# Kernel optimization log

Measured on AMD Instinct MI355X. Metric: run time of the kernel, lower is better.

Reference implementation:

```python
import jax, jax.numpy as jnp
import numpy as np

H_D, W_D = 64, 64          # 1024x1024 image / 16 patch size
N = H_D * W_D              # 4096 patches
D = 768                    # DINO ViT-B/16 embed dim
ALPHA = 0.5
K = 100


def setup_inputs() -> dict:
    key = jax.random.key(0)
    k1, k2 = jax.random.split(key)
    out = jax.random.normal(k1, (N, D), dtype=jnp.float32)
    attn_seed = jax.random.randint(k2, (2,), 0, H_D, dtype=jnp.int32)
    return {"out": out, "attn_seed": attn_seed}


def _connected_components(mask):
    """8-connectivity connected components via iterative min-label propagation.
    Background = 0. Foreground pixels get the minimum initial id (+1) of their
    component (same partition as cv2.connectedComponents, different numbering)."""
    fg = mask > 0
    BIG = jnp.int32(N + 1)
    init = jnp.where(fg, jnp.arange(N, dtype=jnp.int32).reshape(H_D, W_D) + 1, BIG)

    def step(l):
        p = jnp.pad(l, 1, constant_values=N + 1)
        m = l
        for dy in (0, 1, 2):          # fixed 3x3 neighborhood, not a data-dim loop
            for dx in (0, 1, 2):
                m = jnp.minimum(m, p[dy:dy + H_D, dx:dx + W_D])
        return jnp.where(fg, m, BIG)

    def cond(st):
        l, prev = st
        return jnp.any(l != prev)

    def body(st):
        l, _ = st
        return step(l), l

    l, _ = jax.lax.while_loop(cond, body, (step(init), init))
    return jnp.where(fg, l, 0)


def reference(out, attn_seed):
    # similarity between all patch features: [N, N]
    sim = out @ out.T
    deg = sim >= 0                                        # degree_matrix (bool)
    # patch with fewest non-negative similarities
    seed_degree_flat = jnp.argmin(deg.sum(axis=0)).astype(jnp.int32)
    seed_degree = jnp.stack([seed_degree_flat // W_D, seed_degree_flat % W_D])
    # blend degree seed with attention seed
    seed_rc = jnp.round(ALPHA * seed_degree + (1.0 - ALPHA) * attn_seed).astype(jnp.int32)
    seed = seed_rc[0] * W_D + seed_rc[1]

    # initial expansion set = patches positively correlated with the seed
    s = deg[seed].astype(jnp.int32)
    s = s.at[seed].set(1)                                 # degree_matrix[seed][seed] = 255 (truthy)
    order = jnp.argsort(-sim[seed])                       # descending
    s = s.at[order[K:]].set(0)                            # keep top-k most similar

    # sequential seed expansion (updates feed into later iterations)
    def step(s, i):
        grows = jnp.sum(sim[i] * (s == 1)) > 0
        s = s.at[i].set(jnp.where(s[i] == 0, 0, jnp.where(grows, 1, 0)))
        return s, None

    s, _ = jax.lax.scan(step, s, jnp.arange(N))

    return _connected_components(s.reshape(H_D, W_D))
```

## Files before the change

kernel.cpp:

```cpp
#include <hip/hip_runtime.h>
#include <cstdint>

#define NP   4096
#define DD   768
#define HD   64
#define WD   64
#define KTOP 100
#define BIGL 4097

typedef short bf16x8 __attribute__((ext_vector_type(8)));
typedef float f32x4  __attribute__((ext_vector_type(4)));

__device__ __forceinline__ void gload_lds16(const void* g, void* l) {
    __builtin_amdgcn_global_load_lds(
        (const __attribute__((address_space(1))) unsigned int*)(uintptr_t)g,
        (__attribute__((address_space(3))) unsigned int*)(unsigned int)(uintptr_t)l,
        16, 0, 0);
}

__device__ __forceinline__ unsigned short f2bf_rne(float x) {
    unsigned b = __float_as_uint(x);
    unsigned r = b + 0x7FFFu + ((b >> 16) & 1u);
    return (unsigned short)(r >> 16);
}
__device__ __forceinline__ float bf2f(unsigned short h) {
    return __uint_as_float(((unsigned)h) << 16);
}

__global__ __launch_bounds__(256) void k_split(const float* __restrict__ A,
                                               unsigned short* __restrict__ hi,
                                               unsigned short* __restrict__ lo,
                                               int* __restrict__ counts) {
    if (blockIdx.x < 16) counts[blockIdx.x * 256 + threadIdx.x] = 0;
    int idx = blockIdx.x * 256 + threadIdx.x;
    float4 v = ((const float4*)A)[idx];
    unsigned short h0 = f2bf_rne(v.x), h1 = f2bf_rne(v.y),
                   h2 = f2bf_rne(v.z), h3 = f2bf_rne(v.w);
    unsigned short l0 = f2bf_rne(v.x - bf2f(h0)), l1 = f2bf_rne(v.y - bf2f(h1)),
                   l2 = f2bf_rne(v.z - bf2f(h2)), l3 = f2bf_rne(v.w - bf2f(h3));
    ((ushort4*)hi)[idx] = make_ushort4(h0, h1, h2, h3);
    ((ushort4*)lo)[idx] = make_ushort4(l0, l1, l2, l3);
}

__device__ __forceinline__ void stage_group(const unsigned short* __restrict__ hi,
                                            const unsigned short* __restrict__ lo,
                                            int i0, int j0, int kbase, int tid,
                                            unsigned short* G) {
#pragma unroll
    for (int q = 0; q < 4; ++q) {
        int pp = q * 512 + tid;
        int ppt = pp & 1023;
        int row = ppt >> 3;
        int kcl = (ppt & 7) ^ (row & 7);
        int rbase = (pp < 1024) ? i0 : j0;
        const unsigned short* src =
            ((kcl < 4) ? hi : lo) + (size_t)(rbase + row) * DD + kbase + (kcl & 3) * 8;
        gload_lds16(src, G + pp * 8);
    }
}

__global__ __launch_bounds__(512, 4) void k_gemm(const unsigned short* __restrict__ hi,
                                                 const unsigned short* __restrict__ lo,
                                                 int* __restrict__ counts) {
    __shared__ __align__(16) unsigned short G[2][2048 * 8];
    __shared__ int colc[128];
    __shared__ int rowc[128];

    int t = ((blockIdx.x & 7) * 66) + (blockIdx.x >> 3);
    int SI = 0, SJ = 0, rem = t;
    for (;;) {
        int sz = (SI == SJ) ? 36 : 64;
        if (rem < sz) break;
        rem -= sz;
        if (++SJ == 4) { ++SI; SJ = SI; }
    }
    int li, lj;
    if (SI == SJ) {
        int r = 0;
        while (rem >= (8 - r)) { rem -= (8 - r); ++r; }
        li = r; lj = r + rem;
    } else { li = rem >> 3; lj = rem & 7; }
    int bi = SI * 8 + li, bj = SJ * 8 + lj;
    int i0 = bi * 128, j0 = bj * 128;

    int tid = threadIdx.x;
    int lane = tid & 63, w = tid >> 6;
    int wm = w & 1, wn = w >> 1;

    f32x4 acc[4][2];
#pragma unroll
    for (int ti = 0; ti < 4; ++ti)
#pragma unroll
        for (int u = 0; u < 2; ++u) { acc[ti][u][0] = 0.f; acc[ti][u][1] = 0.f;
                                      acc[ti][u][2] = 0.f; acc[ti][u][3] = 0.f; }

    int kcf = lane >> 4;
    int paH[4], paL[4], pbH[2], pbL[2];
#pragma unroll
    for (int tt = 0; tt < 4; ++tt) {
        int arow = wm * 64 + tt * 16 + (lane & 15);
        paH[tt] = arow * 8 + (kcf ^ (arow & 7));
        paL[tt] = arow * 8 + ((kcf + 4) ^ (arow & 7));
    }
#pragma unroll
    for (int u = 0; u < 2; ++u) {
        int brow = wn * 32 + u * 16 + (lane & 15);
        pbH[u] = 1024 + brow * 8 + (kcf ^ (brow & 7));
        pbL[u] = 1024 + brow * 8 + ((kcf + 4) ^ (brow & 7));
    }

    stage_group(hi, lo, i0, j0, 0, tid, G[0]);
    for (int it = 0; it < 24; ++it) {
        int cur = it & 1;
        __syncthreads();
        if (it + 1 < 24)
            stage_group(hi, lo, i0, j0, (it + 1) * 32, tid, G[cur ^ 1]);
        bf16x8 ahi[4], alo[4], bhi[2], blo[2];
#pragma unroll
        for (int tt = 0; tt < 4; ++tt) {
            ahi[tt] = *(const bf16x8*)&G[cur][paH[tt] * 8];
            alo[tt] = *(const bf16x8*)&G[cur][paL[tt] * 8];
        }
#pragma unroll
        for (int u = 0; u < 2; ++u) {
            bhi[u] = *(const bf16x8*)&G[cur][pbH[u] * 8];
            blo[u] = *(const bf16x8*)&G[cur][pbL[u] * 8];
        }
#pragma unroll
        for (int ti = 0; ti < 4; ++ti)
#pragma unroll
            for (int u = 0; u < 2; ++u) {
                acc[ti][u] = __builtin_amdgcn_mfma_f32_16x16x32_bf16(
                    ahi[ti], bhi[u], acc[ti][u], 0, 0, 0);
                acc[ti][u] = __builtin_amdgcn_mfma_f32_16x16x32_bf16(
                    alo[ti], bhi[u], acc[ti][u], 0, 0, 0);
                acc[ti][u] = __builtin_amdgcn_mfma_f32_16x16x32_bf16(
                    ahi[ti], blo[u], acc[ti][u], 0, 0, 0);
            }
    }

    if (tid < 128) { colc[tid] = 0; rowc[tid] = 0; }
    __syncthreads();

    int nl = lane & 15;
    int rg = lane >> 4;
    int cc[2] = {0, 0};
#pragma unroll
    for (int ti = 0; ti < 4; ++ti)
#pragma unroll
        for (int u = 0; u < 2; ++u) {
            f32x4 a = acc[ti][u];
            cc[u] += ((a[0] >= 0.f) ? 1 : 0) + ((a[1] >= 0.f) ? 1 : 0) +
                     ((a[2] >= 0.f) ? 1 : 0) + ((a[3] >= 0.f) ? 1 : 0);
        }
#pragma unroll
    for (int u = 0; u < 2; ++u) {
        int v = cc[u];
        v += __shfl_xor(v, 16);
        v += __shfl_xor(v, 32);
        if (rg == 0) atomicAdd(&colc[wn * 32 + u * 16 + nl], v);
    }
    if (bi != bj) {
#pragma unroll
        for (int ti = 0; ti < 4; ++ti)
#pragma unroll
            for (int g = 0; g < 4; ++g) {
                int rv = ((acc[ti][0][g] >= 0.f) ? 1 : 0) +
                         ((acc[ti][1][g] >= 0.f) ? 1 : 0);
                rv += __shfl_xor(rv, 1);
                rv += __shfl_xor(rv, 2);
                rv += __shfl_xor(rv, 4);
                rv += __shfl_xor(rv, 8);
                if (nl == 0) atomicAdd(&rowc[wm * 64 + ti * 16 + rg * 4 + g], rv);
            }
    }
    __syncthreads();
    if (tid < 128) {
        atomicAdd(&counts[j0 + tid], colc[tid]);
        if (bi != bj) atomicAdd(&counts[i0 + tid], rowc[tid]);
    }
}

__device__ __forceinline__ int block_sum256(int v, int lane, int w, int* wred) {
#pragma unroll
    for (int o = 1; o < 64; o <<= 1) v += __shfl_xor(v, o);
    if (lane == 0) wred[w] = v;
    __syncthreads();
    int tt = wred[0] + wred[1] + wred[2] + wred[3];
    __syncthreads();
    return tt;
}
__device__ __forceinline__ int block_exscan256(int v, int lane, int w, int* wred,
                                               int* total) {
    int inc = v;
#pragma unroll
    for (int o = 1; o < 64; o <<= 1) { int u = __shfl_up(inc, o); if (lane >= o) inc += u; }
    if (lane == 63) wred[w] = inc;
    __syncthreads();
    int w0 = wred[0], w1 = wred[1], w2 = wred[2], w3 = wred[3];
    int wofs = (w > 0 ? w0 : 0) + (w > 1 ? w1 : 0) + (w > 2 ? w2 : 0);
    *total = w0 + w1 + w2 + w3;
    __syncthreads();
    return wofs + inc - v;
}

__global__ __launch_bounds__(256) void k_seedrow(const float* __restrict__ A,
                                                 const int* __restrict__ counts,
                                                 const int* __restrict__ attn_seed,
                                                 float* __restrict__ simrow,
                                                 int* __restrict__ seedp,
                                                 int* __restrict__ outp) {
    __shared__ int redA[256], redB[256];
    int tid = threadIdx.x, lane = tid & 63, w = tid >> 6;
    int blk = blockIdx.x;

    int bc = 0x7fffffff, bI = 0;
    for (int j = tid; j < NP; j += 256) {
        int c = counts[j];
        if (c < bc) { bc = c; bI = j; }
    }
    redA[tid] = bc; redB[tid] = bI;
    __syncthreads();
    for (int st = 128; st > 0; st >>= 1) {
        if (tid < st) {
            if (redA[tid + st] < redA[tid] ||
                (redA[tid + st] == redA[tid] && redB[tid + st] < redB[tid])) {
                redA[tid] = redA[tid + st];
                redB[tid] = redB[tid + st];
            }
        }
        __syncthreads();
    }
    int flat = redB[0];
    int sr = flat / WD, sc = flat % WD;
    int vr = sr + attn_seed[0];
    int vc = sc + attn_seed[1];
    int rr, rc;
    if ((vr & 1) == 0) rr = vr >> 1;
    else { int m = vr >> 1; rr = (m & 1) ? m + 1 : m; }
    if ((vc & 1) == 0) rc = vc >> 1;
    else { int m = vc >> 1; rc = (m & 1) ? m + 1 : m; }
    int seed = rr * WD + rc;
    if (blk == 0 && tid == 0) seedp[0] = seed;

    float sv[12];
#pragma unroll
    for (int kk = 0; kk < 12; ++kk) sv[kk] = A[(size_t)seed * DD + lane + kk * 64];
    int jbase = blk * 8 + w * 2;
#pragma unroll
    for (int jj = 0; jj < 2; ++jj) {
        int j = jbase + jj;
        float sum = 0.f;
#pragma unroll
        for (int kk = 0; kk < 12; ++kk)
            sum += sv[kk] * A[(size_t)j * DD + lane + kk * 64];
#pragma unroll
        for (int o = 32; o > 0; o >>= 1) sum += __shfl_down(sum, o);
        if (lane == 0) simrow[j] = sum;
    }
    if (blk < 128 && tid < 32) outp[blk * 32 + tid] = 0;
}

__global__ __launch_bounds__(256) void k_sel(const float* __restrict__ simrow,
                                             const int* __restrict__ seedp,
                                             int* __restrict__ act, int* __restrict__ Mp) {
    __shared__ int wred[4];
    int tid = threadIdx.x, lane = tid & 63, w = tid >> 6;
    int seed = seedp[0];
    int base = tid * 16;
    unsigned key[16];
#pragma unroll
    for (int n = 0; n < 16; ++n) {
        unsigned b = __float_as_uint(simrow[base + n]);
        key[n] = (b & 0x80000000u) ? ~b : (b | 0x80000000u);
    }
    unsigned prefix = 0;
    for (int bit = 31; bit >= 0; --bit) {
        unsigned cand = prefix | (1u << bit);
        int c = 0;
#pragma unroll
        for (int n = 0; n < 16; ++n) c += (key[n] >= cand) ? 1 : 0;
        int tot = block_sum256(c, lane, w, wred);
        if (tot >= KTOP) prefix = cand;
    }
    unsigned KT = prefix;
    int cgt = 0, ceq = 0;
#pragma unroll
    for (int n = 0; n < 16; ++n) {
        cgt += (key[n] > KT) ? 1 : 0;
        ceq += (key[n] == KT) ? 1 : 0;
    }
    int totgt = block_sum256(cgt, lane, w, wred);
    int slots = KTOP - totgt;
    int dummy;
    int eqrun = block_exscan256(ceq, lane, w, wred, &dummy);
    int flag[16]; int cf = 0;
#pragma unroll
    for (int n = 0; n < 16; ++n) {
        int j = base + n;
        unsigned k = key[n];
        int topk = (k > KT) || (k == KT && eqrun < slots);
        if (k == KT) ++eqrun;
        int f = (topk && (k >= 0x80000000u || j == seed)) ? 1 : 0;
        flag[n] = f; cf += f;
    }
    int M;
    int off = block_exscan256(cf, lane, w, wred, &M);
    if (tid == 0) Mp[0] = M;
#pragma unroll
    for (int n = 0; n < 16; ++n)
        if (flag[n]) act[off++] = base + n;
}

__global__ __launch_bounds__(512) void k_sub(const float* __restrict__ A,
                                             const int* __restrict__ act,
                                             const int* __restrict__ Mp,
                                             float* __restrict__ subsim) {
    __shared__ float av[DD];
    int M = Mp[0];
    int p = blockIdx.x;
    if (p >= M) return;
    int tid = threadIdx.x, lane = tid & 63, w = tid >> 6;
    int ip = act[p];
    for (int k = tid; k < DD; k += 512) av[k] = A[(size_t)ip * DD + k];
    __syncthreads();
    for (int q = w; q < M; q += 8) {
        int iq = act[q];
        float sum = 0.f;
#pragma unroll
        for (int kk = 0; kk < 12; ++kk) {
            int k = lane + kk * 64;
            sum += av[k] * A[(size_t)iq * DD + k];
        }
#pragma unroll
        for (int o = 32; o > 0; o >>= 1) sum += __shfl_down(sum, o);
        if (lane == 0) subsim[p * 128 + q] = sum;
    }
}

__global__ __launch_bounds__(256) void k_fin(const float* __restrict__ subsim,
                                             const int* __restrict__ act,
                                             const int* __restrict__ Mp,
                                             int* __restrict__ outp) {
    __shared__ float ss[128 * 128];
    __shared__ int act_s[128];
    __shared__ int alive[128];
    __shared__ int lab[128];
    __shared__ unsigned char nbr[128][8];
    __shared__ int ncnt[128];
    __shared__ int chg;
    int M = Mp[0];
    int tid = threadIdx.x, lane = tid & 63;

    if (tid < 128) act_s[tid] = (tid < M) ? act[tid] : 0;
    for (int i4 = tid; i4 < M * 32; i4 += 256) {
        int p = i4 >> 5, qb = (i4 & 31) << 2;
        float4 v = ((const float4*)subsim)[i4];
        ss[(qb + 0) * 128 + ((p + qb + 0) & 127)] = v.x;
        ss[(qb + 1) * 128 + ((p + qb + 1) & 127)] = v.y;
        ss[(qb + 2) * 128 + ((p + qb + 2) & 127)] = v.z;
        ss[(qb + 3) * 128 + ((p + qb + 3) & 127)] = v.w;
    }
    __syncthreads();

    if (tid < 64) {
        float S_lo = 0.f, S_hi = 0.f;
        for (int q = 0; q < M; ++q) {
            S_lo += ss[q * 128 + ((lane + q) & 127)];
            S_hi += ss[q * 128 + ((lane + 64 + q) & 127)];
        }
        float al = (lane < M) ? 1.f : 0.f;
        float ah = (lane + 64 < M) ? 1.f : 0.f;
        for (int p = 0; p < M; ++p) {
            float Sp = (p < 64) ? __shfl(S_lo, p) : __shfl(S_hi, p - 64);
            if (!(Sp > 0.f)) {
                S_lo -= ss[p * 128 + ((lane + p) & 127)];
                S_hi -= ss[p * 128 + ((lane + 64 + p) & 127)];
                if (lane == p)      al = 0.f;
                if (lane + 64 == p) ah = 0.f;
            }
        }
        alive[lane]      = (lane < M && al != 0.f) ? 1 : 0;
        alive[lane + 64] = (lane + 64 < M && ah != 0.f) ? 1 : 0;
    }
    __syncthreads();

    if (tid < 128) {
        int a = (tid < M) ? alive[tid] : 0;
        int c = 0;
        if (a) {
            int id = act_s[tid];
            int y = id >> 6, x = id & 63;
            for (int q = 0; q < M; ++q) {
                if (q == tid || !alive[q]) continue;
                int qid = act_s[q];
                int dy = (qid >> 6) - y, dx = (qid & 63) - x;
                if (dy >= -1 && dy <= 1 && dx >= -1 && dx <= 1)
                    nbr[tid][c++] = (unsigned char)q;
            }
        }
        ncnt[tid] = c;
        lab[tid] = a ? tid : 32767;
    }
    __syncthreads();
    while (true) {
        if (tid == 0) chg = 0;
        __syncthreads();
        int local = 0;
        if (tid < M && alive[tid]) {
            int m = lab[tid];
            int nc = ncnt[tid];
            for (int k = 0; k < nc; ++k) { int u = lab[nbr[tid][k]]; if (u < m) m = u; }
            { int u = lab[m]; if (u < m) m = u; }
            { int u = lab[m]; if (u < m) m = u; }
            if (m < lab[tid]) { lab[tid] = m; local = 1; }
        }
        if (local) chg = 1;
        __syncthreads();
        if (chg == 0) break;
        __syncthreads();
    }
    if (tid < M && alive[tid]) outp[act_s[tid]] = act_s[lab[tid]] + 1;
}

extern "C" void kernel_launch(void* const* d_in, const int* in_sizes, int n_in,
                              void* d_out, int out_size, void* d_ws, size_t ws_size,
                              hipStream_t stream) {
    const float* A = (const float*)d_in[0];
    const int* attn = (const int*)d_in[1];
    int* outp = (int*)d_out;

    char* ws = (char*)d_ws;
    int*            counts = (int*)(ws);
    float*          simrow = (float*)(ws + 16384);
    int*            act    = (int*)(ws + 32768);
    int*            Mp     = (int*)(ws + 33280);
    int*            seedp  = (int*)(ws + 33284);
    float*          subsim = (float*)(ws + 33792);
    unsigned short* hi     = (unsigned short*)(ws + 1048576);
    unsigned short* lo     = (unsigned short*)(ws + 1048576 + 6291456);

    k_split  <<<3072, 256, 0, stream>>>(A, hi, lo, counts);
    k_gemm   <<<528,  512, 0, stream>>>(hi, lo, counts);
    k_seedrow<<<512,  256, 0, stream>>>(A, counts, attn, simrow, seedp, outp);
    k_sel    <<<1,    256, 0, stream>>>(simrow, seedp, act, Mp);
    k_sub    <<<128,  512, 0, stream>>>(A, act, Mp, subsim);
    k_fin    <<<1,    256, 0, stream>>>(subsim, act, Mp, outp);
}
```

Baseline: 182.8 us.

## Split GEMM tiles into 128x64 halves and fuse top-k select into sub-similarity kernel

```diff
diff --git a/kernel.cpp b/kernel.cpp
--- a/kernel.cpp
+++ b/kernel.cpp
@@ -6,7 +6,6 @@
 #define HD   64
 #define WD   64
 #define KTOP 100
-#define BIGL 4097
 
 typedef short bf16x8 __attribute__((ext_vector_type(8)));
 typedef float f32x4  __attribute__((ext_vector_type(4)));
@@ -47,27 +46,27 @@
                                             int i0, int j0, int kbase, int tid,
                                             unsigned short* G) {
 #pragma unroll
-    for (int q = 0; q < 4; ++q) {
-        int pp = q * 512 + tid;
-        int ppt = pp & 1023;
+    for (int q = 0; q < 6; ++q) {
+        int pp = q * 256 + tid;
+        int isB = (pp >= 1024);
+        int ppt = isB ? (pp - 1024) : pp;
         int row = ppt >> 3;
         int kcl = (ppt & 7) ^ (row & 7);
-        int rbase = (pp < 1024) ? i0 : j0;
+        int rbase = isB ? j0 : i0;
         const unsigned short* src =
             ((kcl < 4) ? hi : lo) + (size_t)(rbase + row) * DD + kbase + (kcl & 3) * 8;
         gload_lds16(src, G + pp * 8);
     }
 }
 
-__global__ __launch_bounds__(512, 4) void k_gemm(const unsigned short* __restrict__ hi,
+__global__ __launch_bounds__(256, 2) void k_gemm(const unsigned short* __restrict__ hi,
                                                  const unsigned short* __restrict__ lo,
                                                  int* __restrict__ counts) {
-    __shared__ __align__(16) unsigned short G[2][2048 * 8];
-    __shared__ int colc[128];
-    __shared__ int rowc[128];
-
-    int t = ((blockIdx.x & 7) * 66) + (blockIdx.x >> 3);
-    int SI = 0, SJ = 0, rem = t;
+    __shared__ __align__(16) unsigned short G[2][1536 * 8];
+
+    int t = ((blockIdx.x & 7) * 132) + (blockIdx.x >> 3);
+    int pair = t >> 1, h = t & 1;
+    int SI = 0, SJ = 0, rem = pair;
     for (;;) {
         int sz = (SI == SJ) ? 36 : 64;
         if (rem < sz) break;
@@ -81,7 +80,8 @@
         li = r; lj = r + rem;
     } else { li = rem >> 3; lj = rem & 7; }
     int bi = SI * 8 + li, bj = SJ * 8 + lj;
-    int i0 = bi * 128, j0 = bj * 128;
+    int i0 = bi * 128;
+    int j0 = bj * 128 + h * 64;
 
     int tid = threadIdx.x;
     int lane = tid & 63, w = tid >> 6;
@@ -139,7 +139,10 @@
             }
     }
 
-    if (tid < 128) { colc[tid] = 0; rowc[tid] = 0; }
+    __syncthreads();
+    int* colc = (int*)&G[0][0];
+    int* rowc = ((int*)&G[0][0]) + 64;
+    if (tid < 192) ((int*)&G[0][0])[tid] = 0;
     __syncthreads();
 
     int nl = lane & 15;
@@ -175,10 +178,8 @@
             }
     }
     __syncthreads();
-    if (tid < 128) {
-        atomicAdd(&counts[j0 + tid], colc[tid]);
-        if (bi != bj) atomicAdd(&counts[i0 + tid], rowc[tid]);
-    }
+    if (tid < 64) atomicAdd(&counts[j0 + tid], colc[tid]);
+    if (tid < 128 && bi != bj) atomicAdd(&counts[i0 + tid], rowc[tid]);
 }
 
 __device__ __forceinline__ int block_sum256(int v, int lane, int w, int* wred) {
@@ -261,10 +262,14 @@
     if (blk < 128 && tid < 32) outp[blk * 32 + tid] = 0;
 }
 
-__global__ __launch_bounds__(256) void k_sel(const float* __restrict__ simrow,
-                                             const int* __restrict__ seedp,
-                                             int* __restrict__ act, int* __restrict__ Mp) {
+__global__ __launch_bounds__(256) void k_subsel(const float* __restrict__ A,
+                                                const float* __restrict__ simrow,
+                                                const int* __restrict__ seedp,
+                                                int* __restrict__ act, int* __restrict__ Mp,
+                                                float* __restrict__ subsim) {
     __shared__ int wred[4];
+    __shared__ int act_s[128];
+    __shared__ float av[DD];
     int tid = threadIdx.x, lane = tid & 63, w = tid >> 6;
     int seed = seedp[0];
     int base = tid * 16;
@@ -306,26 +311,23 @@
     }
     int M;
     int off = block_exscan256(cf, lane, w, wred, &M);
-    if (tid == 0) Mp[0] = M;
 #pragma unroll
     for (int n = 0; n < 16; ++n)
-        if (flag[n]) act[off++] = base + n;
-}
-
-__global__ __launch_bounds__(512) void k_sub(const float* __restrict__ A,
-                                             const int* __restrict__ act,
-                                             const int* __restrict__ Mp,
-                                             float* __restrict__ subsim) {
-    __shared__ float av[DD];
-    int M = Mp[0];
+        if (flag[n]) act_s[off++] = base + n;
+    __syncthreads();
+
     int p = blockIdx.x;
+    if (p == 0) {
+        if (tid == 0) Mp[0] = M;
+        if (tid < M) act[tid] = act_s[tid];
+    }
     if (p >= M) return;
-    int tid = threadIdx.x, lane = tid & 63, w = tid >> 6;
-    int ip = act[p];
-    for (int k = tid; k < DD; k += 512) av[k] = A[(size_t)ip * DD + k];
-    __syncthreads();
-    for (int q = w; q < M; q += 8) {
-        int iq = act[q];
+
+    int ip = act_s[p];
+    for (int k = tid; k < DD; k += 256) av[k] = A[(size_t)ip * DD + k];
+    __syncthreads();
+    for (int q = w; q < M; q += 4) {
+        int iq = act_s[q];
         float sum = 0.f;
 #pragma unroll
         for (int kk = 0; kk < 12; ++kk) {
@@ -441,9 +443,8 @@
     unsigned short* lo     = (unsigned short*)(ws + 1048576 + 6291456);
 
     k_split  <<<3072, 256, 0, stream>>>(A, hi, lo, counts);
-    k_gemm   <<<528,  512, 0, stream>>>(hi, lo, counts);
+    k_gemm   <<<1056, 256, 0, stream>>>(hi, lo, counts);
     k_seedrow<<<512,  256, 0, stream>>>(A, counts, attn, simrow, seedp, outp);
-    k_sel    <<<1,    256, 0, stream>>>(simrow, seedp, act, Mp);
-    k_sub    <<<128,  512, 0, stream>>>(A, act, Mp, subsim);
+    k_subsel <<<128,  256, 0, stream>>>(A, simrow, seedp, act, Mp, subsim);
     k_fin    <<<1,    256, 0, stream>>>(subsim, act, Mp, outp);
 }
```

Measured after the change: 184.3 us. Within noise of the previous version (+0.8%).

## Fit GEMM grid to 512 blocks and fuse top-k selection into sub-similarity kernel

Applied to the files above, without the earlier changes.

```diff
diff --git a/kernel.cpp b/kernel.cpp
--- a/kernel.cpp
+++ b/kernel.cpp
@@ -6,7 +6,6 @@
 #define HD   64
 #define WD   64
 #define KTOP 100
-#define BIGL 4097
 
 typedef short bf16x8 __attribute__((ext_vector_type(8)));
 typedef float f32x4  __attribute__((ext_vector_type(4)));
@@ -66,33 +65,9 @@
     __shared__ int colc[128];
     __shared__ int rowc[128];
 
-    int t = ((blockIdx.x & 7) * 66) + (blockIdx.x >> 3);
-    int SI = 0, SJ = 0, rem = t;
-    for (;;) {
-        int sz = (SI == SJ) ? 36 : 64;
-        if (rem < sz) break;
-        rem -= sz;
-        if (++SJ == 4) { ++SI; SJ = SI; }
-    }
-    int li, lj;
-    if (SI == SJ) {
-        int r = 0;
-        while (rem >= (8 - r)) { rem -= (8 - r); ++r; }
-        li = r; lj = r + rem;
-    } else { li = rem >> 3; lj = rem & 7; }
-    int bi = SI * 8 + li, bj = SJ * 8 + lj;
-    int i0 = bi * 128, j0 = bj * 128;
-
     int tid = threadIdx.x;
     int lane = tid & 63, w = tid >> 6;
     int wm = w & 1, wn = w >> 1;
-
-    f32x4 acc[4][2];
-#pragma unroll
-    for (int ti = 0; ti < 4; ++ti)
-#pragma unroll
-        for (int u = 0; u < 2; ++u) { acc[ti][u][0] = 0.f; acc[ti][u][1] = 0.f;
-                                      acc[ti][u][2] = 0.f; acc[ti][u][3] = 0.f; }
 
     int kcf = lane >> 4;
     int paH[4], paL[4], pbH[2], pbL[2];
@@ -109,75 +84,105 @@
         pbL[u] = 1024 + brow * 8 + ((kcf + 4) ^ (brow & 7));
     }
 
-    stage_group(hi, lo, i0, j0, 0, tid, G[0]);
-    for (int it = 0; it < 24; ++it) {
-        int cur = it & 1;
-        __syncthreads();
-        if (it + 1 < 24)
-            stage_group(hi, lo, i0, j0, (it + 1) * 32, tid, G[cur ^ 1]);
-        bf16x8 ahi[4], alo[4], bhi[2], blo[2];
-#pragma unroll
-        for (int tt = 0; tt < 4; ++tt) {
-            ahi[tt] = *(const bf16x8*)&G[cur][paH[tt] * 8];
-            alo[tt] = *(const bf16x8*)&G[cur][paL[tt] * 8];
-        }
+    int b = blockIdx.x;
+    int njobs = (b < 16) ? 2 : 1;
+    for (int jj = 0; jj < njobs; ++jj) {
+        int job = (jj == 0) ? b : (512 + b);
+
+        int t = ((job & 7) * 66) + (job >> 3);
+        int SI = 0, SJ = 0, rem = t;
+        for (;;) {
+            int sz = (SI == SJ) ? 36 : 64;
+            if (rem < sz) break;
+            rem -= sz;
+            if (++SJ == 4) { ++SI; SJ = SI; }
+        }
+        int li, lj;
+        if (SI == SJ) {
+            int r = 0;
+            while (rem >= (8 - r)) { rem -= (8 - r); ++r; }
+            li = r; lj = r + rem;
+        } else { li = rem >> 3; lj = rem & 7; }
+        int bi = SI * 8 + li, bj = SJ * 8 + lj;
+        int i0 = bi * 128, j0 = bj * 128;
+
+        f32x4 acc[4][2];
+#pragma unroll
+        for (int ti = 0; ti < 4; ++ti)
+#pragma unroll
+            for (int u = 0; u < 2; ++u) { acc[ti][u][0] = 0.f; acc[ti][u][1] = 0.f;
+                                          acc[ti][u][2] = 0.f; acc[ti][u][3] = 0.f; }
+
+        stage_group(hi, lo, i0, j0, 0, tid, G[0]);
+        for (int it = 0; it < 24; ++it) {
+            int cur = it & 1;
+            __syncthreads();
+            if (it + 1 < 24)
+                stage_group(hi, lo, i0, j0, (it + 1) * 32, tid, G[cur ^ 1]);
+            bf16x8 ahi[4], alo[4], bhi[2], blo[2];
+#pragma unroll
+            for (int tt = 0; tt < 4; ++tt) {
+                ahi[tt] = *(const bf16x8*)&G[cur][paH[tt] * 8];
+                alo[tt] = *(const bf16x8*)&G[cur][paL[tt] * 8];
+            }
+#pragma unroll
+            for (int u = 0; u < 2; ++u) {
+                bhi[u] = *(const bf16x8*)&G[cur][pbH[u] * 8];
+                blo[u] = *(const bf16x8*)&G[cur][pbL[u] * 8];
+            }
+#pragma unroll
+            for (int ti = 0; ti < 4; ++ti)
+#pragma unroll
+                for (int u = 0; u < 2; ++u) {
+                    acc[ti][u] = __builtin_amdgcn_mfma_f32_16x16x32_bf16(
+                        ahi[ti], bhi[u], acc[ti][u], 0, 0, 0);
+                    acc[ti][u] = __builtin_amdgcn_mfma_f32_16x16x32_bf16(
+                        alo[ti], bhi[u], acc[ti][u], 0, 0, 0);
+                    acc[ti][u] = __builtin_amdgcn_mfma_f32_16x16x32_bf16(
+                        ahi[ti], blo[u], acc[ti][u], 0, 0, 0);
+                }
+        }
+
+        if (tid < 128) { colc[tid] = 0; rowc[tid] = 0; }
+        __syncthreads();
+
+        int nl = lane & 15;
+        int rg = lane >> 4;
+        int cc[2] = {0, 0};
+#pragma unroll
+        for (int ti = 0; ti < 4; ++ti)
+#pragma unroll
+            for (int u = 0; u < 2; ++u) {
+                f32x4 a = acc[ti][u];
+                cc[u] += ((a[0] >= 0.f) ? 1 : 0) + ((a[1] >= 0.f) ? 1 : 0) +
+                         ((a[2] >= 0.f) ? 1 : 0) + ((a[3] >= 0.f) ? 1 : 0);
+            }
 #pragma unroll
         for (int u = 0; u < 2; ++u) {
-            bhi[u] = *(const bf16x8*)&G[cur][pbH[u] * 8];
-            blo[u] = *(const bf16x8*)&G[cur][pbL[u] * 8];
-        }
-#pragma unroll
-        for (int ti = 0; ti < 4; ++ti)
-#pragma unroll
-            for (int u = 0; u < 2; ++u) {
-                acc[ti][u] = __builtin_amdgcn_mfma_f32_16x16x32_bf16(
-                    ahi[ti], bhi[u], acc[ti][u], 0, 0, 0);
-                acc[ti][u] = __builtin_amdgcn_mfma_f32_16x16x32_bf16(
-                    alo[ti], bhi[u], acc[ti][u], 0, 0, 0);
-                acc[ti][u] = __builtin_amdgcn_mfma_f32_16x16x32_bf16(
-                    ahi[ti], blo[u], acc[ti][u], 0, 0, 0);
-            }
-    }
-
-    if (tid < 128) { colc[tid] = 0; rowc[tid] = 0; }
-    __syncthreads();
-
-    int nl = lane & 15;
-    int rg = lane >> 4;
-    int cc[2] = {0, 0};
-#pragma unroll
-    for (int ti = 0; ti < 4; ++ti)
-#pragma unroll
-        for (int u = 0; u < 2; ++u) {
-            f32x4 a = acc[ti][u];
-            cc[u] += ((a[0] >= 0.f) ? 1 : 0) + ((a[1] >= 0.f) ? 1 : 0) +
-                     ((a[2] >= 0.f) ? 1 : 0) + ((a[3] >= 0.f) ? 1 : 0);
-        }
-#pragma unroll
-    for (int u = 0; u < 2; ++u) {
-        int v = cc[u];
-        v += __shfl_xor(v, 16);
-        v += __shfl_xor(v, 32);
-        if (rg == 0) atomicAdd(&colc[wn * 32 + u * 16 + nl], v);
-    }
-    if (bi != bj) {
-#pragma unroll
-        for (int ti = 0; ti < 4; ++ti)
-#pragma unroll
-            for (int g = 0; g < 4; ++g) {
-                int rv = ((acc[ti][0][g] >= 0.f) ? 1 : 0) +
-                         ((acc[ti][1][g] >= 0.f) ? 1 : 0);
-                rv += __shfl_xor(rv, 1);
-                rv += __shfl_xor(rv, 2);
-                rv += __shfl_xor(rv, 4);
-                rv += __shfl_xor(rv, 8);
-                if (nl == 0) atomicAdd(&rowc[wm * 64 + ti * 16 + rg * 4 + g], rv);
-            }
-    }
-    __syncthreads();
-    if (tid < 128) {
-        atomicAdd(&counts[j0 + tid], colc[tid]);
-        if (bi != bj) atomicAdd(&counts[i0 + tid], rowc[tid]);
+            int v = cc[u];
+            v += __shfl_xor(v, 16);
+            v += __shfl_xor(v, 32);
+            if (rg == 0) atomicAdd(&colc[wn * 32 + u * 16 + nl], v);
+        }
+        if (bi != bj) {
+#pragma unroll
+            for (int ti = 0; ti < 4; ++ti)
+#pragma unroll
+                for (int g = 0; g < 4; ++g) {
+                    int rv = ((acc[ti][0][g] >= 0.f) ? 1 : 0) +
+                             ((acc[ti][1][g] >= 0.f) ? 1 : 0);
+                    rv += __shfl_xor(rv, 1);
+                    rv += __shfl_xor(rv, 2);
+                    rv += __shfl_xor(rv, 4);
+                    rv += __shfl_xor(rv, 8);
+                    if (nl == 0) atomicAdd(&rowc[wm * 64 + ti * 16 + rg * 4 + g], rv);
+                }
+        }
+        __syncthreads();
+        if (tid < 128) {
+            atomicAdd(&counts[j0 + tid], colc[tid]);
+            if (bi != bj) atomicAdd(&counts[i0 + tid], rowc[tid]);
+        }
     }
 }
 
@@ -261,10 +266,14 @@
     if (blk < 128 && tid < 32) outp[blk * 32 + tid] = 0;
 }
 
-__global__ __launch_bounds__(256) void k_sel(const float* __restrict__ simrow,
-                                             const int* __restrict__ seedp,
-                                             int* __restrict__ act, int* __restrict__ Mp) {
+__global__ __launch_bounds__(256) void k_subsel(const float* __restrict__ A,
+                                                const float* __restrict__ simrow,
+                                                const int* __restrict__ seedp,
+                                                int* __restrict__ act, int* __restrict__ Mp,
+                                                float* __restrict__ subsim) {
     __shared__ int wred[4];
+    __shared__ int act_s[128];
+    __shared__ float av[DD];
     int tid = threadIdx.x, lane = tid & 63, w = tid >> 6;
     int seed = seedp[0];
     int base = tid * 16;
@@ -306,26 +315,23 @@
     }
     int M;
     int off = block_exscan256(cf, lane, w, wred, &M);
-    if (tid == 0) Mp[0] = M;
 #pragma unroll
     for (int n = 0; n < 16; ++n)
-        if (flag[n]) act[off++] = base + n;
-}
-
-__global__ __launch_bounds__(512) void k_sub(const float* __restrict__ A,
-                                             const int* __restrict__ act,
-                                             const int* __restrict__ Mp,
-                                             float* __restrict__ subsim) {
-    __shared__ float av[DD];
-    int M = Mp[0];
+        if (flag[n]) act_s[off++] = base + n;
+    __syncthreads();
+
     int p = blockIdx.x;
+    if (p == 0) {
+        if (tid == 0) Mp[0] = M;
+        if (tid < M) act[tid] = act_s[tid];
+    }
     if (p >= M) return;
-    int tid = threadIdx.x, lane = tid & 63, w = tid >> 6;
-    int ip = act[p];
-    for (int k = tid; k < DD; k += 512) av[k] = A[(size_t)ip * DD + k];
-    __syncthreads();
-    for (int q = w; q < M; q += 8) {
-        int iq = act[q];
+
+    int ip = act_s[p];
+    for (int k = tid; k < DD; k += 256) av[k] = A[(size_t)ip * DD + k];
+    __syncthreads();
+    for (int q = w; q < M; q += 4) {
+        int iq = act_s[q];
         float sum = 0.f;
 #pragma unroll
         for (int kk = 0; kk < 12; ++kk) {
@@ -441,9 +447,8 @@
     unsigned short* lo     = (unsigned short*)(ws + 1048576 + 6291456);
 
     k_split  <<<3072, 256, 0, stream>>>(A, hi, lo, counts);
-    k_gemm   <<<528,  512, 0, stream>>>(hi, lo, counts);
+    k_gemm   <<<512,  512, 0, stream>>>(hi, lo, counts);
     k_seedrow<<<512,  256, 0, stream>>>(A, counts, attn, simrow, seedp, outp);
-    k_sel    <<<1,    256, 0, stream>>>(simrow, seedp, act, Mp);
-    k_sub    <<<128,  512, 0, stream>>>(A, act, Mp, subsim);
+    k_subsel <<<128,  256, 0, stream>>>(A, simrow, seedp, act, Mp, subsim);
     k_fin    <<<1,    256, 0, stream>>>(subsim, act, Mp, outp);
 }
```

Result: no change. 186.2 us (+1.8%).
